# Kernel optimization log

Measured on AMD Instinct MI355X. Metric: run time of the kernel, lower is better.

Reference implementation:

```python
import jax, jax.numpy as jnp
import numpy as np

B, STATE, CTRL, WIDTH = 1024, 64, 16, 128
RTOL = ATOL = 1.4e-8
DT0 = 60.0 * (1.0 / 3600.0)  # dt0 * SECOND, in hours
MAX_STEPS = 128
SAFETY, FMIN, FMAX, EXP = 0.9, 0.1, 10.0, 0.2  # I-controller (diffrax PID default pcoeff=dcoeff=0)

# Tsit5 Butcher tableau
A21 = 0.161
A31, A32 = -0.008480655492356989, 0.335480655492357
A41, A42, A43 = 2.8971530571054935, -6.359448489975075, 4.3622954328695815
A51, A52, A53, A54 = 5.325864828439257, -11.748883564062828, 7.4955393428898365, -0.09249506636175525
A61, A62, A63, A64, A65 = 5.86145544294642, -12.92096931784711, 8.159367898576159, -0.071584973281401, -0.028269050394068383
B1, B2, B3, B4, B5, B6 = 0.09646076681806523, 0.01, 0.4798896504144996, 1.379008574103742, -3.290069515436081, 2.324710524099774
E1, E2, E3, E4, E5, E6, E7 = (-0.001780011052226, -0.000816434459657, 0.007880878010262,
                              -0.144711007173263, 0.582357165452555, -0.458082105929187,
                              -1.0 / 66.0)


def setup_inputs() -> dict:
    key = jax.random.key(0)
    ks = jax.random.split(key, 8)
    def lin(k, fan_in, fan_out):
        kw, kb = jax.random.split(k)
        lim = 1.0 / np.sqrt(fan_in)
        W = jax.random.uniform(kw, (fan_out, fan_in), minval=-lim, maxval=lim, dtype=jnp.float32)
        b = jax.random.uniform(kb, (fan_out,), minval=-lim, maxval=lim, dtype=jnp.float32)
        return W, b
    W0, b0 = lin(ks[0], STATE + CTRL, WIDTH)
    W1, b1 = lin(ks[1], WIDTH, WIDTH)
    W2, b2 = lin(ks[2], WIDTH, STATE)
    x0 = jax.random.normal(ks[3], (B, STATE), dtype=jnp.float32)
    u = jax.random.normal(ks[4], (B, CTRL), dtype=jnp.float32)
    return {"x0": x0, "u": u, "t0": jnp.float32(0.0), "t1": jnp.float32(1.0),
            "W0": W0, "b0": b0, "W1": W1, "b1": b1, "W2": W2, "b2": b2}


def reference(x0, u, t0, t1, W0, b0, W1, b1, W2, b2):
    # vector field f(t, y, u) = MLP(hstack(y, u)); autonomous in t
    def f(y):  # y: [B, STATE] -> [B, STATE]
        z = jnp.concatenate([y, u], axis=-1)
        h = jnp.tanh(z @ W0.T + b0)
        h = jnp.tanh(h @ W1.T + b1)
        return h @ W2.T + b2

    def body(carry, _):
        t, y, dt, nsteps = carry  # t,dt,nsteps: [B]; y: [B,STATE]
        done = t >= t1 - 1e-12
        dt_c = jnp.minimum(dt, t1 - t)          # clip so we don't overshoot t1
        d = dt_c[:, None]
        k1 = f(y)
        k2 = f(y + d * (A21 * k1))
        k3 = f(y + d * (A31 * k1 + A32 * k2))
        k4 = f(y + d * (A41 * k1 + A42 * k2 + A43 * k3))
        k5 = f(y + d * (A51 * k1 + A52 * k2 + A53 * k3 + A54 * k4))
        k6 = f(y + d * (A61 * k1 + A62 * k2 + A63 * k3 + A64 * k4 + A65 * k5))
        y5 = y + d * (B1 * k1 + B2 * k2 + B3 * k3 + B4 * k4 + B5 * k5 + B6 * k6)
        k7 = f(y5)
        err = d * (E1 * k1 + E2 * k2 + E3 * k3 + E4 * k4 + E5 * k5 + E6 * k6 + E7 * k7)
        sc = ATOL + RTOL * jnp.maximum(jnp.abs(y), jnp.abs(y5))
        en = jnp.sqrt(jnp.mean((err / sc) ** 2, axis=-1))      # RMS error norm, [B]
        accept = en <= 1.0
        fac = jnp.clip(SAFETY * jnp.maximum(en, 1e-16) ** (-EXP), FMIN, FMAX)
        step = accept & ~done
        t = jnp.where(step, t + dt_c, t)
        y = jnp.where(step[:, None], y5, y)
        dt = jnp.where(done, dt, dt_c * fac)
        nsteps = nsteps + (~done).astype(jnp.int32)
        return (t, y, dt, nsteps), None

    t = jnp.full((B,), t0, dtype=jnp.float32)
    dt = jnp.full((B,), DT0, dtype=jnp.float32)
    nsteps = jnp.zeros((B,), dtype=jnp.int32)
    (t, y, dt, nsteps), _ = jax.lax.scan(body, (t, x0, dt, nsteps), None, length=MAX_STEPS)
    return y, nsteps  # (sol.ys at t1, ODEMetrics.n_steps)
```

## Files before the change

### kernel.cpp

```cpp
#include <hip/hip_runtime.h>
#include <math.h>

#define TPB 512

#define W0_OFF 0
#define W0_STR 84
#define W1_OFF 10752
#define W1_STR 132
#define W2_OFF 27648
#define W2_STR 132
#define B0_OFF 36096
#define B1_OFF 36224
#define B2_OFF 36352
#define Z_OFF  36416
#define Z_STR  84
#define HA_OFF 36752
#define HB_OFF 37264
#define H_STR  128
#define T_OFF  37776
#define SM_WORDS 37780
#define SM_BYTES (SM_WORDS * 4)

__device__ __forceinline__ float4 ld4(const float* p) {
  return *reinterpret_cast<const float4*>(p);
}

__device__ __forceinline__ float eval_f(float* sm, int tid) {
  const int j = tid & 127;
  const int e = tid >> 7;

  {
    float a = sm[B0_OFF + j];
    const float* wr = sm + W0_OFF + j * W0_STR;
    const float* z  = sm + Z_OFF + e * Z_STR;
#pragma unroll
    for (int i4 = 0; i4 < 20; ++i4) {
      float4 w  = ld4(wr + i4 * 4);
      float4 zz = ld4(z + i4 * 4);
      a = fmaf(w.x, zz.x, a); a = fmaf(w.y, zz.y, a);
      a = fmaf(w.z, zz.z, a); a = fmaf(w.w, zz.w, a);
    }
    sm[HA_OFF + e * H_STR + j] = tanhf(a);
  }
  __syncthreads();

  {
    float a = sm[B1_OFF + j];
    const float* wr = sm + W1_OFF + j * W1_STR;
    const float* z  = sm + HA_OFF + e * H_STR;
#pragma unroll
    for (int i4 = 0; i4 < 32; ++i4) {
      float4 w  = ld4(wr + i4 * 4);
      float4 zz = ld4(z + i4 * 4);
      a = fmaf(w.x, zz.x, a); a = fmaf(w.y, zz.y, a);
      a = fmaf(w.z, zz.z, a); a = fmaf(w.w, zz.w, a);
    }
    sm[HB_OFF + e * H_STR + j] = tanhf(a);
  }
  __syncthreads();

  float a = 0.0f;
  if (tid < 256) {
    const int j3 = tid & 63;
    const int e3 = tid >> 6;
    a = sm[B2_OFF + j3];
    const float* wr = sm + W2_OFF + j3 * W2_STR;
    const float* z  = sm + HB_OFF + e3 * H_STR;
#pragma unroll
    for (int i4 = 0; i4 < 32; ++i4) {
      float4 w  = ld4(wr + i4 * 4);
      float4 zz = ld4(z + i4 * 4);
      a = fmaf(w.x, zz.x, a); a = fmaf(w.y, zz.y, a);
      a = fmaf(w.z, zz.z, a); a = fmaf(w.w, zz.w, a);
    }
  }
  return a;
}

__global__ __launch_bounds__(TPB, 2)
void ode_solver(const float* __restrict__ x0, const float* __restrict__ u,
                const float* __restrict__ t0p, const float* __restrict__ t1p,
                const float* __restrict__ W0g, const float* __restrict__ b0g,
                const float* __restrict__ W1g, const float* __restrict__ b1g,
                const float* __restrict__ W2g, const float* __restrict__ b2g,
                float* __restrict__ out, int B)
{
  extern __shared__ float sm[];
  const int tid = threadIdx.x;
  const int blk = blockIdx.x;

  for (int idx = tid; idx < 128 * 80; idx += TPB) {
    int j = idx / 80, i = idx - j * 80;
    sm[W0_OFF + j * W0_STR + i] = W0g[idx];
  }
  for (int idx = tid; idx < 128 * 128; idx += TPB) {
    int j = idx >> 7, i = idx & 127;
    sm[W1_OFF + j * W1_STR + i] = W1g[idx];
  }
  for (int idx = tid; idx < 64 * 128; idx += TPB) {
    int j = idx >> 7, i = idx & 127;
    sm[W2_OFF + j * W2_STR + i] = W2g[idx];
  }
  if (tid < 128) { sm[B0_OFF + tid] = b0g[tid]; sm[B1_OFF + tid] = b1g[tid]; }
  if (tid < 64)  { sm[B2_OFF + tid] = b2g[tid]; }
  if (tid < 64) {
    int e = tid >> 4, c = tid & 15;
    sm[Z_OFF + e * Z_STR + 64 + c] = u[(blk * 4 + e) * 16 + c];
  }

  const bool own = (tid < 256);
  const int ce = tid >> 6;
  const int cd = tid & 63;
  const int ge = blk * 4 + (ce & 3);

  float y = own ? x0[ge * 64 + cd] : 0.0f;
  const float t1  = *t1p;
  const float t1m = t1 - 1e-12f;
  float tcur = *t0p;
  float dt   = (float)(60.0 * (1.0 / 3600.0));
  int nst = 0;

  constexpr float cA21 = (float)0.161;
  constexpr float cA31 = (float)-0.008480655492356989, cA32 = (float)0.335480655492357;
  constexpr float cA41 = (float)2.8971530571054935,  cA42 = (float)-6.359448489975075,  cA43 = (float)4.3622954328695815;
  constexpr float cA51 = (float)5.325864828439257,   cA52 = (float)-11.748883564062828, cA53 = (float)7.4955393428898365, cA54 = (float)-0.09249506636175525;
  constexpr float cA61 = (float)5.86145544294642,    cA62 = (float)-12.92096931784711,  cA63 = (float)8.159367898576159,  cA64 = (float)-0.071584973281401, cA65 = (float)-0.028269050394068383;
  constexpr float cB1 = (float)0.09646076681806523,  cB2 = (float)0.01, cB3 = (float)0.4798896504144996;
  constexpr float cB4 = (float)1.379008574103742,    cB5 = (float)-3.290069515436081, cB6 = (float)2.324710524099774;
  constexpr float cE1 = (float)-0.001780011052226,   cE2 = (float)-0.000816434459657, cE3 = (float)0.007880878010262;
  constexpr float cE4 = (float)-0.144711007173263,   cE5 = (float)0.582357165452555,  cE6 = (float)-0.458082105929187;
  constexpr float cE7 = (float)(-1.0 / 66.0);

  __syncthreads();

  for (int it = 0; it < 128; ++it) {
    if (own) {
      sm[Z_OFF + ce * Z_STR + cd] = y;
      if (cd == 0) sm[T_OFF + ce] = tcur;
    }
    __syncthreads();
    const bool alldone = (sm[T_OFF + 0] >= t1m) && (sm[T_OFF + 1] >= t1m) &&
                         (sm[T_OFF + 2] >= t1m) && (sm[T_OFF + 3] >= t1m);
    if (alldone) break;

    const bool  done = (tcur >= t1m);
    const float dt_c = fminf(dt, t1 - tcur);
    const float d    = dt_c;

    const float k1 = eval_f(sm, tid);
    float ys = y + d * (cA21 * k1);
    if (own) sm[Z_OFF + ce * Z_STR + cd] = ys;
    __syncthreads();
    const float k2 = eval_f(sm, tid);
    ys = y + d * (cA31 * k1 + cA32 * k2);
    if (own) sm[Z_OFF + ce * Z_STR + cd] = ys;
    __syncthreads();
    const float k3 = eval_f(sm, tid);
    ys = y + d * (cA41 * k1 + cA42 * k2 + cA43 * k3);
    if (own) sm[Z_OFF + ce * Z_STR + cd] = ys;
    __syncthreads();
    const float k4 = eval_f(sm, tid);
    ys = y + d * (cA51 * k1 + cA52 * k2 + cA53 * k3 + cA54 * k4);
    if (own) sm[Z_OFF + ce * Z_STR + cd] = ys;
    __syncthreads();
    const float k5 = eval_f(sm, tid);
    ys = y + d * (cA61 * k1 + cA62 * k2 + cA63 * k3 + cA64 * k4 + cA65 * k5);
    if (own) sm[Z_OFF + ce * Z_STR + cd] = ys;
    __syncthreads();
    const float k6 = eval_f(sm, tid);
    const float y5v = y + d * (cB1 * k1 + cB2 * k2 + cB3 * k3 + cB4 * k4 + cB5 * k5 + cB6 * k6);
    if (own) sm[Z_OFF + ce * Z_STR + cd] = y5v;
    __syncthreads();
    const float k7 = eval_f(sm, tid);

    const float err = d * (cE1 * k1 + cE2 * k2 + cE3 * k3 + cE4 * k4 + cE5 * k5 + cE6 * k6 + cE7 * k7);
    const float sc  = 1.4e-8f + 1.4e-8f * fmaxf(fabsf(y), fabsf(y5v));
    const float r   = err / sc;
    float s2 = r * r;
#pragma unroll
    for (int m = 1; m < 64; m <<= 1) s2 += __shfl_xor(s2, m);
    const float en = sqrtf(s2 * (1.0f / 64.0f));

    const bool accept = (en <= 1.0f);
    float fac = 0.9f * powf(fmaxf(en, 1e-16f), -0.2f);
    fac = fminf(10.0f, fmaxf(0.1f, fac));
    const bool step = accept && !done;
    if (step) { tcur = tcur + dt_c; y = y5v; }
    if (!done) dt = dt_c * fac;
    nst += done ? 0 : 1;
  }

  if (own) {
    out[ge * 64 + cd] = y;
    if (cd == 0) out[B * 64 + ge] = (float)nst;
  }
}

extern "C" void kernel_launch(void* const* d_in, const int* in_sizes, int n_in,
                              void* d_out, int out_size, void* d_ws, size_t ws_size,
                              hipStream_t stream) {
  const float* x0 = (const float*)d_in[0];
  const float* u  = (const float*)d_in[1];
  const float* t0 = (const float*)d_in[2];
  const float* t1 = (const float*)d_in[3];
  const float* W0 = (const float*)d_in[4];
  const float* b0 = (const float*)d_in[5];
  const float* W1 = (const float*)d_in[6];
  const float* b1 = (const float*)d_in[7];
  const float* W2 = (const float*)d_in[8];
  const float* b2 = (const float*)d_in[9];
  float* out = (float*)d_out;

  const int B = in_sizes[0] / 64;
  const int nblk = B / 4;

  (void)hipFuncSetAttribute((const void*)ode_solver,
                            hipFuncAttributeMaxDynamicSharedMemorySize, SM_BYTES);
  ode_solver<<<nblk, TPB, SM_BYTES, stream>>>(x0, u, t0, t1, W0, b0, W1, b1, W2, b2, out, B);
}
```

Baseline: 2.758 ms.

## Give each wavefront two batch elements and drop block-wide barriers in MLP eval

Restructures the ODE solver so each 64-lane wavefront owns two batch elements end-to-end. It computes all three MLP layers for them using wavefront-private shared-memory scratch, with 2x2 register blocking that reuses each weight and activation load. This removes every __syncthreads from the RK stages and lets each wavefront stop early once both of its elements are done. Blocks shrink to 256 threads with 8 elements each, so there are half as many blocks and more shared memory per block, which may lower occupancy and load balance. It also relies on implicit wavefront lockstep for the shared-memory handoffs between layers.

Result: slower. 9.546 ms (+246.1%).

```diff
diff --git a/kernel.cpp b/kernel.cpp
--- a/kernel.cpp
+++ b/kernel.cpp
@@ -1,7 +1,7 @@
 #include <hip/hip_runtime.h>
 #include <math.h>
 
-#define TPB 512
+#define TPB 256
 
 #define W0_OFF 0
 #define W0_STR 84
@@ -14,70 +14,97 @@
 #define B2_OFF 36352
 #define Z_OFF  36416
 #define Z_STR  84
-#define HA_OFF 36752
-#define HB_OFF 37264
+#define HA_OFF 37088
+#define HB_OFF 38112
 #define H_STR  128
-#define T_OFF  37776
-#define SM_WORDS 37780
+#define SM_WORDS 39136
 #define SM_BYTES (SM_WORDS * 4)
 
 __device__ __forceinline__ float4 ld4(const float* p) {
   return *reinterpret_cast<const float4*>(p);
 }
 
-__device__ __forceinline__ float eval_f(float* sm, int tid) {
-  const int j = tid & 127;
-  const int e = tid >> 7;
-
+__device__ __forceinline__ void eval_f2(const float* __restrict__ sm,
+                                        float* hA1, float* hB1,
+                                        float* hA2, float* hB2,
+                                        const float* zA, const float* zB,
+                                        int lane, float& kA, float& kB)
+{
   {
-    float a = sm[B0_OFF + j];
-    const float* wr = sm + W0_OFF + j * W0_STR;
-    const float* z  = sm + Z_OFF + e * Z_STR;
+    float a00 = sm[B0_OFF + lane];
+    float a01 = a00;
+    float a10 = sm[B0_OFF + lane + 64];
+    float a11 = a10;
+    const float* w0a = sm + W0_OFF + lane * W0_STR;
+    const float* w0b = sm + W0_OFF + (lane + 64) * W0_STR;
 #pragma unroll
     for (int i4 = 0; i4 < 20; ++i4) {
-      float4 w  = ld4(wr + i4 * 4);
-      float4 zz = ld4(z + i4 * 4);
-      a = fmaf(w.x, zz.x, a); a = fmaf(w.y, zz.y, a);
-      a = fmaf(w.z, zz.z, a); a = fmaf(w.w, zz.w, a);
-    }
-    sm[HA_OFF + e * H_STR + j] = tanhf(a);
-  }
-  __syncthreads();
+      float4 wa = ld4(w0a + i4 * 4);
+      float4 wb = ld4(w0b + i4 * 4);
+      float4 za = ld4(zA + i4 * 4);
+      float4 zb = ld4(zB + i4 * 4);
+      a00 = fmaf(wa.x, za.x, a00); a00 = fmaf(wa.y, za.y, a00);
+      a00 = fmaf(wa.z, za.z, a00); a00 = fmaf(wa.w, za.w, a00);
+      a01 = fmaf(wa.x, zb.x, a01); a01 = fmaf(wa.y, zb.y, a01);
+      a01 = fmaf(wa.z, zb.z, a01); a01 = fmaf(wa.w, zb.w, a01);
+      a10 = fmaf(wb.x, za.x, a10); a10 = fmaf(wb.y, za.y, a10);
+      a10 = fmaf(wb.z, za.z, a10); a10 = fmaf(wb.w, za.w, a10);
+      a11 = fmaf(wb.x, zb.x, a11); a11 = fmaf(wb.y, zb.y, a11);
+      a11 = fmaf(wb.z, zb.z, a11); a11 = fmaf(wb.w, zb.w, a11);
+    }
+    hA1[lane]      = tanhf(a00);
+    hB1[lane]      = tanhf(a01);
+    hA1[lane + 64] = tanhf(a10);
+    hB1[lane + 64] = tanhf(a11);
+  }
 
   {
-    float a = sm[B1_OFF + j];
-    const float* wr = sm + W1_OFF + j * W1_STR;
-    const float* z  = sm + HA_OFF + e * H_STR;
+    float a00 = sm[B1_OFF + lane];
+    float a01 = a00;
+    float a10 = sm[B1_OFF + lane + 64];
+    float a11 = a10;
+    const float* w1a = sm + W1_OFF + lane * W1_STR;
+    const float* w1b = sm + W1_OFF + (lane + 64) * W1_STR;
 #pragma unroll
     for (int i4 = 0; i4 < 32; ++i4) {
-      float4 w  = ld4(wr + i4 * 4);
-      float4 zz = ld4(z + i4 * 4);
-      a = fmaf(w.x, zz.x, a); a = fmaf(w.y, zz.y, a);
-      a = fmaf(w.z, zz.z, a); a = fmaf(w.w, zz.w, a);
-    }
-    sm[HB_OFF + e * H_STR + j] = tanhf(a);
-  }
-  __syncthreads();
-
-  float a = 0.0f;
-  if (tid < 256) {
-    const int j3 = tid & 63;
-    const int e3 = tid >> 6;
-    a = sm[B2_OFF + j3];
-    const float* wr = sm + W2_OFF + j3 * W2_STR;
-    const float* z  = sm + HB_OFF + e3 * H_STR;
+      float4 wa = ld4(w1a + i4 * 4);
+      float4 wb = ld4(w1b + i4 * 4);
+      float4 za = ld4(hA1 + i4 * 4);
+      float4 zb = ld4(hB1 + i4 * 4);
+      a00 = fmaf(wa.x, za.x, a00); a00 = fmaf(wa.y, za.y, a00);
+      a00 = fmaf(wa.z, za.z, a00); a00 = fmaf(wa.w, za.w, a00);
+      a01 = fmaf(wa.x, zb.x, a01); a01 = fmaf(wa.y, zb.y, a01);
+      a01 = fmaf(wa.z, zb.z, a01); a01 = fmaf(wa.w, zb.w, a01);
+      a10 = fmaf(wb.x, za.x, a10); a10 = fmaf(wb.y, za.y, a10);
+      a10 = fmaf(wb.z, za.z, a10); a10 = fmaf(wb.w, za.w, a10);
+      a11 = fmaf(wb.x, zb.x, a11); a11 = fmaf(wb.y, zb.y, a11);
+      a11 = fmaf(wb.z, zb.z, a11); a11 = fmaf(wb.w, zb.w, a11);
+    }
+    hA2[lane]      = tanhf(a00);
+    hB2[lane]      = tanhf(a01);
+    hA2[lane + 64] = tanhf(a10);
+    hB2[lane + 64] = tanhf(a11);
+  }
+
+  {
+    float aA = sm[B2_OFF + lane];
+    float aB = aA;
+    const float* w2 = sm + W2_OFF + lane * W2_STR;
 #pragma unroll
     for (int i4 = 0; i4 < 32; ++i4) {
-      float4 w  = ld4(wr + i4 * 4);
-      float4 zz = ld4(z + i4 * 4);
-      a = fmaf(w.x, zz.x, a); a = fmaf(w.y, zz.y, a);
-      a = fmaf(w.z, zz.z, a); a = fmaf(w.w, zz.w, a);
-    }
-  }
-  return a;
-}
-
-__global__ __launch_bounds__(TPB, 2)
+      float4 w  = ld4(w2 + i4 * 4);
+      float4 za = ld4(hA2 + i4 * 4);
+      float4 zb = ld4(hB2 + i4 * 4);
+      aA = fmaf(w.x, za.x, aA); aA = fmaf(w.y, za.y, aA);
+      aA = fmaf(w.z, za.z, aA); aA = fmaf(w.w, za.w, aA);
+      aB = fmaf(w.x, zb.x, aB); aB = fmaf(w.y, zb.y, aB);
+      aB = fmaf(w.z, zb.z, aB); aB = fmaf(w.w, zb.w, aB);
+    }
+    kA = aA; kB = aB;
+  }
+}
+
+__global__ __launch_bounds__(TPB, 1)
 void ode_solver(const float* __restrict__ x0, const float* __restrict__ u,
                 const float* __restrict__ t0p, const float* __restrict__ t1p,
                 const float* __restrict__ W0g, const float* __restrict__ b0g,
@@ -103,22 +130,23 @@
   }
   if (tid < 128) { sm[B0_OFF + tid] = b0g[tid]; sm[B1_OFF + tid] = b1g[tid]; }
   if (tid < 64)  { sm[B2_OFF + tid] = b2g[tid]; }
-  if (tid < 64) {
+  if (tid < 128) {
     int e = tid >> 4, c = tid & 15;
-    sm[Z_OFF + e * Z_STR + 64 + c] = u[(blk * 4 + e) * 16 + c];
-  }
-
-  const bool own = (tid < 256);
-  const int ce = tid >> 6;
-  const int cd = tid & 63;
-  const int ge = blk * 4 + (ce & 3);
-
-  float y = own ? x0[ge * 64 + cd] : 0.0f;
+    sm[Z_OFF + e * Z_STR + 64 + c] = u[(blk * 8 + e) * 16 + c];
+  }
+
+  const int wv   = tid >> 6;
+  const int lane = tid & 63;
+  const int eA = 2 * wv, eB = 2 * wv + 1;
+  const int geA = blk * 8 + eA, geB = blk * 8 + eB;
+
+  float yA = x0[geA * 64 + lane];
+  float yB = x0[geB * 64 + lane];
   const float t1  = *t1p;
   const float t1m = t1 - 1e-12f;
-  float tcur = *t0p;
-  float dt   = (float)(60.0 * (1.0 / 3600.0));
-  int nst = 0;
+  float tA = *t0p, tB = tA;
+  float dtA = (float)(60.0 * (1.0 / 3600.0)), dtB = dtA;
+  int nstA = 0, nstB = 0;
 
   constexpr float cA21 = (float)0.161;
   constexpr float cA31 = (float)-0.008480655492356989, cA32 = (float)0.335480655492357;
@@ -133,66 +161,87 @@
 
   __syncthreads();
 
+  float* zA  = sm + Z_OFF + eA * Z_STR;
+  float* zB  = sm + Z_OFF + eB * Z_STR;
+  float* hA1 = sm + HA_OFF + eA * H_STR;
+  float* hB1 = sm + HA_OFF + eB * H_STR;
+  float* hA2 = sm + HB_OFF + eA * H_STR;
+  float* hB2 = sm + HB_OFF + eB * H_STR;
+
   for (int it = 0; it < 128; ++it) {
-    if (own) {
-      sm[Z_OFF + ce * Z_STR + cd] = y;
-      if (cd == 0) sm[T_OFF + ce] = tcur;
-    }
-    __syncthreads();
-    const bool alldone = (sm[T_OFF + 0] >= t1m) && (sm[T_OFF + 1] >= t1m) &&
-                         (sm[T_OFF + 2] >= t1m) && (sm[T_OFF + 3] >= t1m);
-    if (alldone) break;
-
-    const bool  done = (tcur >= t1m);
-    const float dt_c = fminf(dt, t1 - tcur);
-    const float d    = dt_c;
-
-    const float k1 = eval_f(sm, tid);
-    float ys = y + d * (cA21 * k1);
-    if (own) sm[Z_OFF + ce * Z_STR + cd] = ys;
-    __syncthreads();
-    const float k2 = eval_f(sm, tid);
-    ys = y + d * (cA31 * k1 + cA32 * k2);
-    if (own) sm[Z_OFF + ce * Z_STR + cd] = ys;
-    __syncthreads();
-    const float k3 = eval_f(sm, tid);
-    ys = y + d * (cA41 * k1 + cA42 * k2 + cA43 * k3);
-    if (own) sm[Z_OFF + ce * Z_STR + cd] = ys;
-    __syncthreads();
-    const float k4 = eval_f(sm, tid);
-    ys = y + d * (cA51 * k1 + cA52 * k2 + cA53 * k3 + cA54 * k4);
-    if (own) sm[Z_OFF + ce * Z_STR + cd] = ys;
-    __syncthreads();
-    const float k5 = eval_f(sm, tid);
-    ys = y + d * (cA61 * k1 + cA62 * k2 + cA63 * k3 + cA64 * k4 + cA65 * k5);
-    if (own) sm[Z_OFF + ce * Z_STR + cd] = ys;
-    __syncthreads();
-    const float k6 = eval_f(sm, tid);
-    const float y5v = y + d * (cB1 * k1 + cB2 * k2 + cB3 * k3 + cB4 * k4 + cB5 * k5 + cB6 * k6);
-    if (own) sm[Z_OFF + ce * Z_STR + cd] = y5v;
-    __syncthreads();
-    const float k7 = eval_f(sm, tid);
-
-    const float err = d * (cE1 * k1 + cE2 * k2 + cE3 * k3 + cE4 * k4 + cE5 * k5 + cE6 * k6 + cE7 * k7);
-    const float sc  = 1.4e-8f + 1.4e-8f * fmaxf(fabsf(y), fabsf(y5v));
-    const float r   = err / sc;
-    float s2 = r * r;
-#pragma unroll
-    for (int m = 1; m < 64; m <<= 1) s2 += __shfl_xor(s2, m);
-    const float en = sqrtf(s2 * (1.0f / 64.0f));
-
-    const bool accept = (en <= 1.0f);
-    float fac = 0.9f * powf(fmaxf(en, 1e-16f), -0.2f);
-    fac = fminf(10.0f, fmaxf(0.1f, fac));
-    const bool step = accept && !done;
-    if (step) { tcur = tcur + dt_c; y = y5v; }
-    if (!done) dt = dt_c * fac;
-    nst += done ? 0 : 1;
-  }
-
-  if (own) {
-    out[ge * 64 + cd] = y;
-    if (cd == 0) out[B * 64 + ge] = (float)nst;
+    const bool doneA = (tA >= t1m);
+    const bool doneB = (tB >= t1m);
+    if (doneA && doneB) break;
+
+    const float dA = fminf(dtA, t1 - tA);
+    const float dB = fminf(dtB, t1 - tB);
+
+    float k1A, k1B, k2A, k2B, k3A, k3B, k4A, k4B, k5A, k5B, k6A, k6B, k7A, k7B;
+
+    zA[lane] = yA;  zB[lane] = yB;
+    eval_f2(sm, hA1, hB1, hA2, hB2, zA, zB, lane, k1A, k1B);
+
+    zA[lane] = yA + dA * (cA21 * k1A);
+    zB[lane] = yB + dB * (cA21 * k1B);
+    eval_f2(sm, hA1, hB1, hA2, hB2, zA, zB, lane, k2A, k2B);
+
+    zA[lane] = yA + dA * (cA31 * k1A + cA32 * k2A);
+    zB[lane] = yB + dB * (cA31 * k1B + cA32 * k2B);
+    eval_f2(sm, hA1, hB1, hA2, hB2, zA, zB, lane, k3A, k3B);
+
+    zA[lane] = yA + dA * (cA41 * k1A + cA42 * k2A + cA43 * k3A);
+    zB[lane] = yB + dB * (cA41 * k1B + cA42 * k2B + cA43 * k3B);
+    eval_f2(sm, hA1, hB1, hA2, hB2, zA, zB, lane, k4A, k4B);
+
+    zA[lane] = yA + dA * (cA51 * k1A + cA52 * k2A + cA53 * k3A + cA54 * k4A);
+    zB[lane] = yB + dB * (cA51 * k1B + cA52 * k2B + cA53 * k3B + cA54 * k4B);
+    eval_f2(sm, hA1, hB1, hA2, hB2, zA, zB, lane, k5A, k5B);
+
+    zA[lane] = yA + dA * (cA61 * k1A + cA62 * k2A + cA63 * k3A + cA64 * k4A + cA65 * k5A);
+    zB[lane] = yB + dB * (cA61 * k1B + cA62 * k2B + cA63 * k3B + cA64 * k4B + cA65 * k5B);
+    eval_f2(sm, hA1, hB1, hA2, hB2, zA, zB, lane, k6A, k6B);
+
+    const float y5A = yA + dA * (cB1 * k1A + cB2 * k2A + cB3 * k3A + cB4 * k4A + cB5 * k5A + cB6 * k6A);
+    const float y5B = yB + dB * (cB1 * k1B + cB2 * k2B + cB3 * k3B + cB4 * k4B + cB5 * k5B + cB6 * k6B);
+    zA[lane] = y5A;  zB[lane] = y5B;
+    eval_f2(sm, hA1, hB1, hA2, hB2, zA, zB, lane, k7A, k7B);
+
+    const float errA = dA * (cE1 * k1A + cE2 * k2A + cE3 * k3A + cE4 * k4A + cE5 * k5A + cE6 * k6A + cE7 * k7A);
+    const float errB = dB * (cE1 * k1B + cE2 * k2B + cE3 * k3B + cE4 * k4B + cE5 * k5B + cE6 * k6B + cE7 * k7B);
+    const float scA = 1.4e-8f + 1.4e-8f * fmaxf(fabsf(yA), fabsf(y5A));
+    const float scB = 1.4e-8f + 1.4e-8f * fmaxf(fabsf(yB), fabsf(y5B));
+    const float rA = errA / scA;
+    const float rB = errB / scB;
+    float s2A = rA * rA;
+    float s2B = rB * rB;
+#pragma unroll
+    for (int m = 1; m < 64; m <<= 1) {
+      s2A += __shfl_xor(s2A, m);
+      s2B += __shfl_xor(s2B, m);
+    }
+    const float enA = sqrtf(s2A * (1.0f / 64.0f));
+    const float enB = sqrtf(s2B * (1.0f / 64.0f));
+
+    float facA = 0.9f * powf(fmaxf(enA, 1e-16f), -0.2f);
+    float facB = 0.9f * powf(fmaxf(enB, 1e-16f), -0.2f);
+    facA = fminf(10.0f, fmaxf(0.1f, facA));
+    facB = fminf(10.0f, fmaxf(0.1f, facB));
+
+    const bool stepA = (enA <= 1.0f) && !doneA;
+    const bool stepB = (enB <= 1.0f) && !doneB;
+    if (stepA) { tA = tA + dA; yA = y5A; }
+    if (stepB) { tB = tB + dB; yB = y5B; }
+    if (!doneA) dtA = dA * facA;
+    if (!doneB) dtB = dB * facB;
+    nstA += doneA ? 0 : 1;
+    nstB += doneB ? 0 : 1;
+  }
+
+  out[geA * 64 + lane] = yA;
+  out[geB * 64 + lane] = yB;
+  if (lane == 0) {
+    out[B * 64 + geA] = (float)nstA;
+    out[B * 64 + geB] = (float)nstB;
   }
 }
 
@@ -212,7 +261,7 @@
   float* out = (float*)d_out;
 
   const int B = in_sizes[0] / 64;
-  const int nblk = B / 4;
+  const int nblk = B / 8;
 
   (void)hipFuncSetAttribute((const void*)ode_solver,
                             hipFuncAttributeMaxDynamicSharedMemorySize, SM_BYTES);
```
